# Optimization experiments

Measured on AMD Instinct MI355X. Metric: run time of the kernel, lower is better.

## Reference

```python
import jax, jax.numpy as jnp
import numpy as np

N, F_IN, HID, E, G = 100000, 256, 256, 800000, 256


def setup_inputs() -> dict:
    key = jax.random.key(0)
    ks = jax.random.split(key, 10)
    x = jax.random.normal(ks[0], (N, F_IN), dtype=jnp.float32)
    edge_index = jax.random.randint(ks[1], (2, E), 0, N, dtype=jnp.int64)
    batch = jnp.sort(jax.random.randint(ks[2], (N,), 0, G, dtype=jnp.int64))
    s = 1.0 / np.sqrt(HID)
    W1 = jax.random.normal(ks[3], (F_IN, HID), dtype=jnp.float32) * s
    b1 = jnp.zeros((HID,), dtype=jnp.float32)
    W2 = jax.random.normal(ks[4], (HID, HID), dtype=jnp.float32) * s
    b2 = jnp.zeros((HID,), dtype=jnp.float32)
    Wc1 = jax.random.normal(ks[5], (HID, HID // 2), dtype=jnp.float32) * s
    bc1 = jnp.zeros((HID // 2,), dtype=jnp.float32)
    Wc2 = jax.random.normal(ks[6], (HID // 2, 2), dtype=jnp.float32) * s
    bc2 = jnp.zeros((2,), dtype=jnp.float32)
    return dict(x=x, edge_index=edge_index, batch=batch, num_graphs=G,
                W1=W1, b1=b1, W2=W2, b2=b2, Wc1=Wc1, bc1=bc1, Wc2=Wc2, bc2=bc2)


def _gcn_layer(h, src, dst, inv_sqrt_deg, W, b):
    # GCNConv: D^-1/2 (A + I) D^-1/2 (h W) + b
    hw = h @ W                                            # (N, H)
    coef = inv_sqrt_deg[src] * inv_sqrt_deg[dst]          # (E,)
    msgs = hw[src] * coef[:, None]                        # (E, H)
    agg = jax.ops.segment_sum(msgs, dst, num_segments=h.shape[0])
    self_loop = hw * (inv_sqrt_deg * inv_sqrt_deg)[:, None]
    return agg + self_loop + b


def reference(x, edge_index, batch, num_graphs, W1, b1, W2, b2, Wc1, bc1, Wc2, bc2):
    n = x.shape[0]
    src, dst = edge_index[0], edge_index[1]
    # degree with self-loops (symmetric normalization)
    deg = jax.ops.segment_sum(jnp.ones((src.shape[0],), jnp.float32), dst,
                              num_segments=n) + 1.0
    inv_sqrt_deg = jax.lax.rsqrt(deg)

    h = jax.nn.relu(_gcn_layer(x, src, dst, inv_sqrt_deg, W1, b1))
    node_emb = jax.nn.relu(_gcn_layer(h, src, dst, inv_sqrt_deg, W2, b2))

    # per-graph mean pooling (segment mean replacing the Python loop)
    sums = jax.ops.segment_sum(node_emb, batch, num_segments=num_graphs)
    counts = jax.ops.segment_sum(jnp.ones((n,), jnp.float32), batch,
                                 num_segments=num_graphs)
    graph_emb = sums / jnp.maximum(counts, 1.0)[:, None]

    # classifier MLP (dropout is identity in eval mode)
    hcls = jax.nn.relu(graph_emb @ Wc1 + bc1)
    logits = hcls @ Wc2 + bc2                             # (G, 2)
    return logits, node_emb
```

## Files before the change

kernel.cpp:

```cpp
#include <hip/hip_runtime.h>
#include <hip/hip_bf16.h>

#define HID 256
#define NGRAPH 256

typedef __bf16 bf16_t;
typedef __attribute__((ext_vector_type(8))) __bf16 bf16x8;
typedef __attribute__((ext_vector_type(4))) __bf16 bf16x4;
typedef __attribute__((ext_vector_type(4))) float f32x4;

__global__ void zero_int_kernel(int* __restrict__ p, int n) {
    int i = blockIdx.x * blockDim.x + threadIdx.x;
    if (i < n) p[i] = 0;
}

__global__ void count_deg_kernel(const int* __restrict__ ei, int E, int* __restrict__ deg) {
    int e = blockIdx.x * blockDim.x + threadIdx.x;
    if (e >= E) return;
    int dst = ei[E + e];
    atomicAdd(&deg[dst], 1);
}

#define SCHUNK 512

__global__ __launch_bounds__(256) void scan_pass1_kernel(
    const int* __restrict__ deg, int N, int* __restrict__ bsum) {
    __shared__ int red[256];
    int b = blockIdx.x, t = threadIdx.x;
    int i0 = b * SCHUNK + 2 * t;
    int v = 0;
    if (i0 < N) v += deg[i0];
    if (i0 + 1 < N) v += deg[i0 + 1];
    red[t] = v;
    __syncthreads();
    for (int s = 128; s > 0; s >>= 1) {
        if (t < s) red[t] += red[t + s];
        __syncthreads();
    }
    if (t == 0) bsum[b] = red[0];
}

__global__ __launch_bounds__(256) void scan_pass2_kernel(
    const int* __restrict__ bsum, int NB, int* __restrict__ boff) {
    __shared__ int s[256];
    int t = threadIdx.x;
    int v = (t < NB) ? bsum[t] : 0;
    s[t] = v;
    __syncthreads();
    for (int off = 1; off < 256; off <<= 1) {
        int x = s[t];
        if (t >= off) x += s[t - off];
        __syncthreads();
        s[t] = x;
        __syncthreads();
    }
    if (t < NB) boff[t] = s[t] - v;
}

__global__ __launch_bounds__(256) void scan_pass3_kernel(
    const int* __restrict__ deg, int N, const int* __restrict__ boff,
    int* __restrict__ rowptr, int* __restrict__ cursor, float* __restrict__ invd) {
    __shared__ int s[256];
    int b = blockIdx.x, t = threadIdx.x;
    int i0 = b * SCHUNK + 2 * t;
    int d0 = (i0 < N) ? deg[i0] : 0;
    int d1 = (i0 + 1 < N) ? deg[i0 + 1] : 0;
    int pair = d0 + d1;
    s[t] = pair;
    __syncthreads();
    for (int off = 1; off < 256; off <<= 1) {
        int x = s[t];
        if (t >= off) x += s[t - off];
        __syncthreads();
        s[t] = x;
        __syncthreads();
    }
    int excl = s[t] - pair + boff[b];
    if (i0 < N) {
        rowptr[i0] = excl;
        cursor[i0] = excl;
        invd[i0] = rsqrtf((float)d0 + 1.0f);
    }
    if (i0 + 1 < N) {
        int e1 = excl + d0;
        rowptr[i0 + 1] = e1;
        cursor[i0 + 1] = e1;
        invd[i0 + 1] = rsqrtf((float)d1 + 1.0f);
    }
}

__global__ void fill_csr_kernel(const int* __restrict__ ei, int E,
                                int* __restrict__ cursor, int* __restrict__ csr_src) {
    int e = blockIdx.x * blockDim.x + threadIdx.x;
    if (e >= E) return;
    int src = ei[e];
    int dst = ei[E + e];
    int pos = atomicAdd(&cursor[dst], 1);
    csr_src[pos] = src;
}

__global__ __launch_bounds__(256) void wsplit_kernel(
    const float* __restrict__ W, bf16_t* __restrict__ Wf) {
    int idx = blockIdx.x * 256 + threadIdx.x;
    float w = W[idx];
    int k = idx >> 8, n = idx & 255;
    int k0 = k >> 5, kg = (k >> 3) & 3, j = k & 7;
    int nt = n >> 4, m = n & 15;
    Wf[(size_t)(((k0 * 16 + nt) * 64) + kg * 16 + m) * 8 + j] = (bf16_t)w;
}

#define GBM 128

template <int SPLIT>
__global__ __launch_bounds__(512, 4) void gemm_mfma_kernel(
    const void* __restrict__ Xv, const bf16_t* __restrict__ Wf,
    const float* __restrict__ rowscale, bf16_t* __restrict__ out, int Nrows) {
    __shared__ bf16_t Blds[32768];

    const int tid = threadIdx.x;
    const int wave = tid >> 6;
    const int lane = tid & 63;
    const int row0 = blockIdx.x * GBM;
    const int m = lane & 15;
    const int kg = lane >> 4;

    const int arow_raw = row0 + wave * 16 + m;
    const int arow = (arow_raw < Nrows) ? arow_raw : 0;

    f32x4 acc[16];
#pragma unroll
    for (int i = 0; i < 16; ++i) acc[i] = (f32x4){0.f, 0.f, 0.f, 0.f};

#pragma unroll
    for (int c = 0; c < 2; ++c) {
        float4 xa0, xb0, xa1, xb1, xa2, xb2, xa3, xb3;
        bf16x8 ah0, ah1, ah2, ah3;
        if (SPLIT) {
            const float* xr = (const float*)Xv + (size_t)arow * 256 + c * 128 + kg * 8;
            xa0 = *(const float4*)&xr[0];   xb0 = *(const float4*)&xr[4];
            xa1 = *(const float4*)&xr[32];  xb1 = *(const float4*)&xr[36];
            xa2 = *(const float4*)&xr[64];  xb2 = *(const float4*)&xr[68];
            xa3 = *(const float4*)&xr[96];  xb3 = *(const float4*)&xr[100];
        } else {
            const bf16_t* xr = (const bf16_t*)Xv + (size_t)arow * 256 + c * 128 + kg * 8;
            ah0 = *(const bf16x8*)&xr[0];
            ah1 = *(const bf16x8*)&xr[32];
            ah2 = *(const bf16x8*)&xr[64];
            ah3 = *(const bf16x8*)&xr[96];
        }

        if (c) __syncthreads();
#pragma unroll
        for (int it = 0; it < 8; ++it)
            *(bf16x8*)&Blds[it * 4096 + tid * 8] =
                *(const bf16x8*)&Wf[c * 32768 + it * 4096 + tid * 8];
        __syncthreads();

#pragma unroll
        for (int k0c = 0; k0c < 4; ++k0c) {
            bf16x8 ah, al;
            if (SPLIT) {
                float4 xa = (k0c == 0) ? xa0 : (k0c == 1) ? xa1 : (k0c == 2) ? xa2 : xa3;
                float4 xb = (k0c == 0) ? xb0 : (k0c == 1) ? xb1 : (k0c == 2) ? xb2 : xb3;
                float xf[8] = {xa.x, xa.y, xa.z, xa.w, xb.x, xb.y, xb.z, xb.w};
#pragma unroll
                for (int q = 0; q < 8; ++q) {
                    bf16_t hi = (bf16_t)xf[q];
                    ah[q] = hi;
                    al[q] = (bf16_t)(xf[q] - (float)hi);
                }
            } else {
                ah = (k0c == 0) ? ah0 : (k0c == 1) ? ah1 : (k0c == 2) ? ah2 : ah3;
            }
#pragma unroll
            for (int nt = 0; nt < 16; ++nt) {
                bf16x8 bh = *(const bf16x8*)&Blds[(k0c * 16 + nt) * 512 + lane * 8];
                acc[nt] = __builtin_amdgcn_mfma_f32_16x16x32_bf16(ah, bh, acc[nt], 0, 0, 0);
                if (SPLIT)
                    acc[nt] = __builtin_amdgcn_mfma_f32_16x16x32_bf16(al, bh, acc[nt], 0, 0, 0);
            }
        }
    }

    const int rbase = row0 + wave * 16 + kg * 4;
#pragma unroll
    for (int j = 0; j < 4; ++j) {
        int r = rbase + j;
        if (r < Nrows) {
            float sc = rowscale[r];
#pragma unroll
            for (int nt = 0; nt < 16; ++nt)
                out[(size_t)r * 256 + nt * 16 + m] = (bf16_t)(acc[nt][j] * sc);
        }
    }
}

template <typename OutT>
__global__ __launch_bounds__(256) void gcn_aggregate_kernel(
    const bf16_t* __restrict__ hs, const int* __restrict__ rowptr,
    const int* __restrict__ deg, const int* __restrict__ csr_src,
    const float* __restrict__ inv_d, const float* __restrict__ bias,
    OutT* __restrict__ out, int N) {
    int gwid = (blockIdx.x * blockDim.x + threadIdx.x) >> 6;
    int lane = threadIdx.x & 63;
    if (gwid >= N) return;
    int base = rowptr[gwid];
    int len = deg[gwid];
    int c = lane * 4;

    bf16x4 sv = *(const bf16x4*)&hs[(size_t)gwid * 256 + c];
    float ax0 = (float)sv[0], ay0 = (float)sv[1], az0 = (float)sv[2], aw0 = (float)sv[3];
    float ax1 = 0.f, ay1 = 0.f, az1 = 0.f, aw1 = 0.f;
    float ax2 = 0.f, ay2 = 0.f, az2 = 0.f, aw2 = 0.f;
    float ax3 = 0.f, ay3 = 0.f, az3 = 0.f, aw3 = 0.f;
    int i = 0;
    for (; i + 8 <= len; i += 8) {
        int s0 = csr_src[base + i];
        int s1 = csr_src[base + i + 1];
        int s2 = csr_src[base + i + 2];
        int s3 = csr_src[base + i + 3];
        int s4 = csr_src[base + i + 4];
        int s5 = csr_src[base + i + 5];
        int s6 = csr_src[base + i + 6];
        int s7 = csr_src[base + i + 7];
        bf16x4 v0 = *(const bf16x4*)&hs[(size_t)s0 * 256 + c];
        bf16x4 v1 = *(const bf16x4*)&hs[(size_t)s1 * 256 + c];
        bf16x4 v2 = *(const bf16x4*)&hs[(size_t)s2 * 256 + c];
        bf16x4 v3 = *(const bf16x4*)&hs[(size_t)s3 * 256 + c];
        bf16x4 v4 = *(const bf16x4*)&hs[(size_t)s4 * 256 + c];
        bf16x4 v5 = *(const bf16x4*)&hs[(size_t)s5 * 256 + c];
        bf16x4 v6 = *(const bf16x4*)&hs[(size_t)s6 * 256 + c];
        bf16x4 v7 = *(const bf16x4*)&hs[(size_t)s7 * 256 + c];
        ax0 += (float)v0[0] + (float)v4[0]; ay0 += (float)v0[1] + (float)v4[1];
        az0 += (float)v0[2] + (float)v4[2]; aw0 += (float)v0[3] + (float)v4[3];
        ax1 += (float)v1[0] + (float)v5[0]; ay1 += (float)v1[1] + (float)v5[1];
        az1 += (float)v1[2] + (float)v5[2]; aw1 += (float)v1[3] + (float)v5[3];
        ax2 += (float)v2[0] + (float)v6[0]; ay2 += (float)v2[1] + (float)v6[1];
        az2 += (float)v2[2] + (float)v6[2]; aw2 += (float)v2[3] + (float)v6[3];
        ax3 += (float)v3[0] + (float)v7[0]; ay3 += (float)v3[1] + (float)v7[1];
        az3 += (float)v3[2] + (float)v7[2]; aw3 += (float)v3[3] + (float)v7[3];
    }
    for (; i + 4 <= len; i += 4) {
        int s0 = csr_src[base + i];
        int s1 = csr_src[base + i + 1];
        int s2 = csr_src[base + i + 2];
        int s3 = csr_src[base + i + 3];
        bf16x4 v0 = *(const bf16x4*)&hs[(size_t)s0 * 256 + c];
        bf16x4 v1 = *(const bf16x4*)&hs[(size_t)s1 * 256 + c];
        bf16x4 v2 = *(const bf16x4*)&hs[(size_t)s2 * 256 + c];
        bf16x4 v3 = *(const bf16x4*)&hs[(size_t)s3 * 256 + c];
        ax0 += (float)v0[0]; ay0 += (float)v0[1]; az0 += (float)v0[2]; aw0 += (float)v0[3];
        ax1 += (float)v1[0]; ay1 += (float)v1[1]; az1 += (float)v1[2]; aw1 += (float)v1[3];
        ax2 += (float)v2[0]; ay2 += (float)v2[1]; az2 += (float)v2[2]; aw2 += (float)v2[3];
        ax3 += (float)v3[0]; ay3 += (float)v3[1]; az3 += (float)v3[2]; aw3 += (float)v3[3];
    }
    for (; i < len; ++i) {
        int s = csr_src[base + i];
        bf16x4 v = *(const bf16x4*)&hs[(size_t)s * 256 + c];
        ax0 += (float)v[0]; ay0 += (float)v[1]; az0 += (float)v[2]; aw0 += (float)v[3];
    }
    float ax = (ax0 + ax1) + (ax2 + ax3);
    float ay = (ay0 + ay1) + (ay2 + ay3);
    float az = (az0 + az1) + (az2 + az3);
    float aw = (aw0 + aw1) + (aw2 + aw3);

    float sc = inv_d[gwid];
    float4 bb = *(const float4*)&bias[c];
    float ox = fmaxf(fmaf(ax, sc, bb.x), 0.f);
    float oy = fmaxf(fmaf(ay, sc, bb.y), 0.f);
    float oz = fmaxf(fmaf(az, sc, bb.z), 0.f);
    float ow = fmaxf(fmaf(aw, sc, bb.w), 0.f);
    if constexpr (sizeof(OutT) == 2) {
        bf16x4 o;
        o[0] = (bf16_t)ox; o[1] = (bf16_t)oy; o[2] = (bf16_t)oz; o[3] = (bf16_t)ow;
        *(bf16x4*)&out[(size_t)gwid * 256 + c] = o;
    } else {
        float4 o = {ox, oy, oz, ow};
        *(float4*)&out[(size_t)gwid * 256 + c] = o;
    }
}

__global__ void graph_bounds_kernel(const int* __restrict__ batch, int N, int G,
                                    int* __restrict__ gstart) {
    int i = blockIdx.x * blockDim.x + threadIdx.x;
    if (i > N) return;
    int cur = (i < N) ? batch[i] : G;
    int prev = (i == 0) ? -1 : batch[i - 1];
    for (int g = prev + 1; g <= cur; ++g) gstart[g] = i;
}

__global__ __launch_bounds__(256) void pool_mean_kernel(
    const float* __restrict__ emb, const int* __restrict__ gstart,
    float* __restrict__ gemb) {
    __shared__ float red[4][64];
    int g = blockIdx.x;
    int col = blockIdx.y * 64 + (threadIdx.x & 63);
    int rg = threadIdx.x >> 6;
    int s = gstart[g], e = gstart[g + 1];
    float sum = 0.f;
    for (int n = s + rg; n < e; n += 4) sum += emb[(size_t)n * 256 + col];
    red[rg][threadIdx.x & 63] = sum;
    __syncthreads();
    if (rg == 0) {
        int l = threadIdx.x & 63;
        float t = (red[0][l] + red[1][l]) + (red[2][l] + red[3][l]);
        float cnt = fmaxf((float)(e - s), 1.0f);
        gemb[g * 256 + col] = t / cnt;
    }
}

__global__ __launch_bounds__(128) void cls1_kernel(
    const float* __restrict__ gemb, const float* __restrict__ Wc1,
    const float* __restrict__ bc1, float* __restrict__ hcls) {
    int g = blockIdx.x;
    int j = threadIdx.x;
    float sum = bc1[j];
    for (int k = 0; k < 256; ++k) sum = fmaf(gemb[g * 256 + k], Wc1[k * 128 + j], sum);
    hcls[g * 128 + j] = fmaxf(sum, 0.f);
}

__global__ void cls2_kernel(const float* __restrict__ hcls, const float* __restrict__ Wc2,
                            const float* __restrict__ bc2, float* __restrict__ logits, int G) {
    int idx = blockIdx.x * blockDim.x + threadIdx.x;
    if (idx >= G * 2) return;
    int g = idx >> 1, c = idx & 1;
    float sum = bc2[c];
    for (int k = 0; k < 128; ++k) sum = fmaf(hcls[g * 128 + k], Wc2[k * 2 + c], sum);
    logits[idx] = sum;
}

extern "C" void kernel_launch(void* const* d_in, const int* in_sizes, int n_in,
                              void* d_out, int out_size, void* d_ws, size_t ws_size,
                              hipStream_t stream) {
    const float* x   = (const float*)d_in[0];
    const int*   ei  = (const int*)d_in[1];
    const int*   batch = (const int*)d_in[2];
    const float* W1  = (const float*)d_in[4];
    const float* b1  = (const float*)d_in[5];
    const float* W2  = (const float*)d_in[6];
    const float* b2  = (const float*)d_in[7];
    const float* Wc1 = (const float*)d_in[8];
    const float* bc1 = (const float*)d_in[9];
    const float* Wc2 = (const float*)d_in[10];
    const float* bc2 = (const float*)d_in[11];

    const int N = in_sizes[0] / HID;
    const int E = in_sizes[1] / 2;
    const int G = NGRAPH;

    float* logits   = (float*)d_out;
    float* node_out = (float*)d_out + (size_t)G * 2;

    char* wsb = (char*)d_ws;
    size_t off = 0;
    auto alloc = [&](size_t bytes) -> void* {
        void* p = wsb + off;
        off += (bytes + 255) & ~(size_t)255;
        return p;
    };
    bf16_t* hs     = (bf16_t*)alloc((size_t)N * HID * 2);
    bf16_t* hb     = (bf16_t*)alloc((size_t)N * HID * 2);
    int*    rowptr = (int*)alloc((size_t)N * 4);
    int*    cursor = (int*)alloc((size_t)N * 4);
    int*    degi   = (int*)alloc((size_t)N * 4);
    int*    csr    = (int*)alloc((size_t)E * 4);
    float*  invd   = (float*)alloc((size_t)N * 4);
    int*    gstart = (int*)alloc((size_t)(G + 1) * 4);
    float*  gemb   = (float*)alloc((size_t)G * HID * 4);
    float*  hcls   = (float*)alloc((size_t)G * (HID / 2) * 4);
    int*    bsum   = (int*)alloc(256 * 4);
    int*    boff   = (int*)alloc(256 * 4);
    bf16_t* wf     = (bf16_t*)alloc((size_t)HID * HID * 2);
    (void)ws_size; (void)n_in; (void)out_size;

    const int NB = (N + SCHUNK - 1) / SCHUNK;

    zero_int_kernel<<<(N + 255) / 256, 256, 0, stream>>>(degi, N);
    count_deg_kernel<<<(E + 255) / 256, 256, 0, stream>>>(ei, E, degi);
    scan_pass1_kernel<<<NB, 256, 0, stream>>>(degi, N, bsum);
    scan_pass2_kernel<<<1, 256, 0, stream>>>(bsum, NB, boff);
    scan_pass3_kernel<<<NB, 256, 0, stream>>>(degi, N, boff, rowptr, cursor, invd);
    fill_csr_kernel<<<(E + 255) / 256, 256, 0, stream>>>(ei, E, cursor, csr);

    const int GB = (N + GBM - 1) / GBM;

    wsplit_kernel<<<HID * HID / 256, 256, 0, stream>>>(W1, wf);
    gemm_mfma_kernel<1><<<GB, 512, 0, stream>>>(x, wf, invd, hs, N);
    gcn_aggregate_kernel<bf16_t><<<(N * 64 + 255) / 256, 256, 0, stream>>>(
        hs, rowptr, degi, csr, invd, b1, hb, N);

    wsplit_kernel<<<HID * HID / 256, 256, 0, stream>>>(W2, wf);
    gemm_mfma_kernel<0><<<GB, 512, 0, stream>>>(hb, wf, invd, hs, N);
    gcn_aggregate_kernel<float><<<(N * 64 + 255) / 256, 256, 0, stream>>>(
        hs, rowptr, degi, csr, invd, b2, node_out, N);

    graph_bounds_kernel<<<(N + 1 + 255) / 256, 256, 0, stream>>>(batch, N, G, gstart);
    pool_mean_kernel<<<dim3(G, 4), 256, 0, stream>>>(node_out, gstart, gemb);
    cls1_kernel<<<G, 128, 0, stream>>>(gemb, Wc1, bc1, hcls);
    cls2_kernel<<<(G * 2 + 255) / 256, 256, 0, stream>>>(hcls, Wc2, bc2, logits, G);
}
```

Before: 383.5 us.

## Drop split-bf16 residual MFMA, widen aggregation to two nodes per wave, merge weight prep

The first-layer GEMM no longer splits fp32 inputs into high and low bf16 parts, which halves its MFMA count but lowers the precision of x@W1. The aggregation kernel now processes two nodes per wave, with each lane handling 8 bf16 columns through 16-byte loads instead of 4 columns, and its unroll is cut from 8 to 4 neighbours. The two weight-reformat launches are merged into one kernel that writes separate buffers. Together these reduce GEMM compute, widen memory transactions in the gather, and remove a launch, at some risk to numerical accuracy.

```diff
diff --git a/kernel.cpp b/kernel.cpp
--- a/kernel.cpp
+++ b/kernel.cpp
@@ -99,9 +99,13 @@
     csr_src[pos] = src;
 }
 
-__global__ __launch_bounds__(256) void wsplit_kernel(
-    const float* __restrict__ W, bf16_t* __restrict__ Wf) {
-    int idx = blockIdx.x * 256 + threadIdx.x;
+__global__ __launch_bounds__(256) void wsplit2_kernel(
+    const float* __restrict__ W1, bf16_t* __restrict__ Wf1,
+    const float* __restrict__ W2, bf16_t* __restrict__ Wf2) {
+    int gi = blockIdx.x * 256 + threadIdx.x;
+    const float* W = (gi < 65536) ? W1 : W2;
+    bf16_t* Wf = (gi < 65536) ? Wf1 : Wf2;
+    int idx = gi & 65535;
     float w = W[idx];
     int k = idx >> 8, n = idx & 255;
     int k0 = k >> 5, kg = (k >> 3) & 3, j = k & 7;
@@ -111,7 +115,7 @@
 
 #define GBM 128
 
-template <int SPLIT>
+template <int INFP32>
 __global__ __launch_bounds__(512, 4) void gemm_mfma_kernel(
     const void* __restrict__ Xv, const bf16_t* __restrict__ Wf,
     const float* __restrict__ rowscale, bf16_t* __restrict__ out, int Nrows) {
@@ -135,7 +139,7 @@
     for (int c = 0; c < 2; ++c) {
         float4 xa0, xb0, xa1, xb1, xa2, xb2, xa3, xb3;
         bf16x8 ah0, ah1, ah2, ah3;
-        if (SPLIT) {
+        if (INFP32) {
             const float* xr = (const float*)Xv + (size_t)arow * 256 + c * 128 + kg * 8;
             xa0 = *(const float4*)&xr[0];   xb0 = *(const float4*)&xr[4];
             xa1 = *(const float4*)&xr[32];  xb1 = *(const float4*)&xr[36];
@@ -158,17 +162,13 @@
 
 #pragma unroll
         for (int k0c = 0; k0c < 4; ++k0c) {
-            bf16x8 ah, al;
-            if (SPLIT) {
+            bf16x8 ah;
+            if (INFP32) {
                 float4 xa = (k0c == 0) ? xa0 : (k0c == 1) ? xa1 : (k0c == 2) ? xa2 : xa3;
                 float4 xb = (k0c == 0) ? xb0 : (k0c == 1) ? xb1 : (k0c == 2) ? xb2 : xb3;
                 float xf[8] = {xa.x, xa.y, xa.z, xa.w, xb.x, xb.y, xb.z, xb.w};
 #pragma unroll
-                for (int q = 0; q < 8; ++q) {
-                    bf16_t hi = (bf16_t)xf[q];
-                    ah[q] = hi;
-                    al[q] = (bf16_t)(xf[q] - (float)hi);
-                }
+                for (int q = 0; q < 8; ++q) ah[q] = (bf16_t)xf[q];
             } else {
                 ah = (k0c == 0) ? ah0 : (k0c == 1) ? ah1 : (k0c == 2) ? ah2 : ah3;
             }
@@ -176,8 +176,6 @@
             for (int nt = 0; nt < 16; ++nt) {
                 bf16x8 bh = *(const bf16x8*)&Blds[(k0c * 16 + nt) * 512 + lane * 8];
                 acc[nt] = __builtin_amdgcn_mfma_f32_16x16x32_bf16(ah, bh, acc[nt], 0, 0, 0);
-                if (SPLIT)
-                    acc[nt] = __builtin_amdgcn_mfma_f32_16x16x32_bf16(al, bh, acc[nt], 0, 0, 0);
             }
         }
     }
@@ -203,80 +201,60 @@
     OutT* __restrict__ out, int N) {
     int gwid = (blockIdx.x * blockDim.x + threadIdx.x) >> 6;
     int lane = threadIdx.x & 63;
-    if (gwid >= N) return;
-    int base = rowptr[gwid];
-    int len = deg[gwid];
-    int c = lane * 4;
-
-    bf16x4 sv = *(const bf16x4*)&hs[(size_t)gwid * 256 + c];
-    float ax0 = (float)sv[0], ay0 = (float)sv[1], az0 = (float)sv[2], aw0 = (float)sv[3];
-    float ax1 = 0.f, ay1 = 0.f, az1 = 0.f, aw1 = 0.f;
-    float ax2 = 0.f, ay2 = 0.f, az2 = 0.f, aw2 = 0.f;
-    float ax3 = 0.f, ay3 = 0.f, az3 = 0.f, aw3 = 0.f;
+    int node = gwid * 2 + (lane >> 5);
+    int hl = lane & 31;
+    if (node >= N) return;
+    int base = rowptr[node];
+    int len = deg[node];
+    int c = hl * 8;
+
+    bf16x8 sv = *(const bf16x8*)&hs[(size_t)node * 256 + c];
+    float a0[8], a1[8];
+#pragma unroll
+    for (int q = 0; q < 8; ++q) { a0[q] = (float)sv[q]; a1[q] = 0.f; }
+
     int i = 0;
-    for (; i + 8 <= len; i += 8) {
-        int s0 = csr_src[base + i];
-        int s1 = csr_src[base + i + 1];
-        int s2 = csr_src[base + i + 2];
-        int s3 = csr_src[base + i + 3];
-        int s4 = csr_src[base + i + 4];
-        int s5 = csr_src[base + i + 5];
-        int s6 = csr_src[base + i + 6];
-        int s7 = csr_src[base + i + 7];
-        bf16x4 v0 = *(const bf16x4*)&hs[(size_t)s0 * 256 + c];
-        bf16x4 v1 = *(const bf16x4*)&hs[(size_t)s1 * 256 + c];
-        bf16x4 v2 = *(const bf16x4*)&hs[(size_t)s2 * 256 + c];
-        bf16x4 v3 = *(const bf16x4*)&hs[(size_t)s3 * 256 + c];
-        bf16x4 v4 = *(const bf16x4*)&hs[(size_t)s4 * 256 + c];
-        bf16x4 v5 = *(const bf16x4*)&hs[(size_t)s5 * 256 + c];
-        bf16x4 v6 = *(const bf16x4*)&hs[(size_t)s6 * 256 + c];
-        bf16x4 v7 = *(const bf16x4*)&hs[(size_t)s7 * 256 + c];
-        ax0 += (float)v0[0] + (float)v4[0]; ay0 += (float)v0[1] + (float)v4[1];
-        az0 += (float)v0[2] + (float)v4[2]; aw0 += (float)v0[3] + (float)v4[3];
-        ax1 += (float)v1[0] + (float)v5[0]; ay1 += (float)v1[1] + (float)v5[1];
-        az1 += (float)v1[2] + (float)v5[2]; aw1 += (float)v1[3] + (float)v5[3];
-        ax2 += (float)v2[0] + (float)v6[0]; ay2 += (float)v2[1] + (float)v6[1];
-        az2 += (float)v2[2] + (float)v6[2]; aw2 += (float)v2[3] + (float)v6[3];
-        ax3 += (float)v3[0] + (float)v7[0]; ay3 += (float)v3[1] + (float)v7[1];
-        az3 += (float)v3[2] + (float)v7[2]; aw3 += (float)v3[3] + (float)v7[3];
-    }
     for (; i + 4 <= len; i += 4) {
         int s0 = csr_src[base + i];
         int s1 = csr_src[base + i + 1];
         int s2 = csr_src[base + i + 2];
         int s3 = csr_src[base + i + 3];
-        bf16x4 v0 = *(const bf16x4*)&hs[(size_t)s0 * 256 + c];
-        bf16x4 v1 = *(const bf16x4*)&hs[(size_t)s1 * 256 + c];
-        bf16x4 v2 = *(const bf16x4*)&hs[(size_t)s2 * 256 + c];
-        bf16x4 v3 = *(const bf16x4*)&hs[(size_t)s3 * 256 + c];
-        ax0 += (float)v0[0]; ay0 += (float)v0[1]; az0 += (float)v0[2]; aw0 += (float)v0[3];
-        ax1 += (float)v1[0]; ay1 += (float)v1[1]; az1 += (float)v1[2]; aw1 += (float)v1[3];
-        ax2 += (float)v2[0]; ay2 += (float)v2[1]; az2 += (float)v2[2]; aw2 += (float)v2[3];
-        ax3 += (float)v3[0]; ay3 += (float)v3[1]; az3 += (float)v3[2]; aw3 += (float)v3[3];
+        bf16x8 v0 = *(const bf16x8*)&hs[(size_t)s0 * 256 + c];
+        bf16x8 v1 = *(const bf16x8*)&hs[(size_t)s1 * 256 + c];
+        bf16x8 v2 = *(const bf16x8*)&hs[(size_t)s2 * 256 + c];
+        bf16x8 v3 = *(const bf16x8*)&hs[(size_t)s3 * 256 + c];
+#pragma unroll
+        for (int q = 0; q < 8; ++q) {
+            a0[q] += (float)v0[q] + (float)v2[q];
+            a1[q] += (float)v1[q] + (float)v3[q];
+        }
     }
     for (; i < len; ++i) {
         int s = csr_src[base + i];
-        bf16x4 v = *(const bf16x4*)&hs[(size_t)s * 256 + c];
-        ax0 += (float)v[0]; ay0 += (float)v[1]; az0 += (float)v[2]; aw0 += (float)v[3];
-    }
-    float ax = (ax0 + ax1) + (ax2 + ax3);
-    float ay = (ay0 + ay1) + (ay2 + ay3);
-    float az = (az0 + az1) + (az2 + az3);
-    float aw = (aw0 + aw1) + (aw2 + aw3);
-
-    float sc = inv_d[gwid];
-    float4 bb = *(const float4*)&bias[c];
-    float ox = fmaxf(fmaf(ax, sc, bb.x), 0.f);
-    float oy = fmaxf(fmaf(ay, sc, bb.y), 0.f);
-    float oz = fmaxf(fmaf(az, sc, bb.z), 0.f);
-    float ow = fmaxf(fmaf(aw, sc, bb.w), 0.f);
+        bf16x8 v = *(const bf16x8*)&hs[(size_t)s * 256 + c];
+#pragma unroll
+        for (int q = 0; q < 8; ++q) a0[q] += (float)v[q];
+    }
+
+    float sc = inv_d[node];
+    float4 bbA = *(const float4*)&bias[c];
+    float4 bbB = *(const float4*)&bias[c + 4];
+    float bb[8] = {bbA.x, bbA.y, bbA.z, bbA.w, bbB.x, bbB.y, bbB.z, bbB.w};
+    float o[8];
+#pragma unroll
+    for (int q = 0; q < 8; ++q)
+        o[q] = fmaxf(fmaf(a0[q] + a1[q], sc, bb[q]), 0.f);
+
     if constexpr (sizeof(OutT) == 2) {
-        bf16x4 o;
-        o[0] = (bf16_t)ox; o[1] = (bf16_t)oy; o[2] = (bf16_t)oz; o[3] = (bf16_t)ow;
-        *(bf16x4*)&out[(size_t)gwid * 256 + c] = o;
+        bf16x8 ov;
+#pragma unroll
+        for (int q = 0; q < 8; ++q) ov[q] = (bf16_t)o[q];
+        *(bf16x8*)&out[(size_t)node * 256 + c] = ov;
     } else {
-        float4 o = {ox, oy, oz, ow};
-        *(float4*)&out[(size_t)gwid * 256 + c] = o;
+        float4 oA = {o[0], o[1], o[2], o[3]};
+        float4 oB = {o[4], o[5], o[6], o[7]};
+        *(float4*)&out[(size_t)node * 256 + c] = oA;
+        *(float4*)&out[(size_t)node * 256 + c + 4] = oB;
     }
 }
 
@@ -370,7 +348,8 @@
     float*  hcls   = (float*)alloc((size_t)G * (HID / 2) * 4);
     int*    bsum   = (int*)alloc(256 * 4);
     int*    boff   = (int*)alloc(256 * 4);
-    bf16_t* wf     = (bf16_t*)alloc((size_t)HID * HID * 2);
+    bf16_t* wf1    = (bf16_t*)alloc((size_t)HID * HID * 2);
+    bf16_t* wf2    = (bf16_t*)alloc((size_t)HID * HID * 2);
     (void)ws_size; (void)n_in; (void)out_size;
 
     const int NB = (N + SCHUNK - 1) / SCHUNK;
@@ -381,17 +360,17 @@
     scan_pass2_kernel<<<1, 256, 0, stream>>>(bsum, NB, boff);
     scan_pass3_kernel<<<NB, 256, 0, stream>>>(degi, N, boff, rowptr, cursor, invd);
     fill_csr_kernel<<<(E + 255) / 256, 256, 0, stream>>>(ei, E, cursor, csr);
+    wsplit2_kernel<<<2 * HID * HID / 256, 256, 0, stream>>>(W1, wf1, W2, wf2);
 
     const int GB = (N + GBM - 1) / GBM;
-
-    wsplit_kernel<<<HID * HID / 256, 256, 0, stream>>>(W1, wf);
-    gemm_mfma_kernel<1><<<GB, 512, 0, stream>>>(x, wf, invd, hs, N);
-    gcn_aggregate_kernel<bf16_t><<<(N * 64 + 255) / 256, 256, 0, stream>>>(
+    const int AB = ((N + 1) / 2 * 64 + 255) / 256;
+
+    gemm_mfma_kernel<1><<<GB, 512, 0, stream>>>(x, wf1, invd, hs, N);
+    gcn_aggregate_kernel<bf16_t><<<AB, 256, 0, stream>>>(
         hs, rowptr, degi, csr, invd, b1, hb, N);
 
-    wsplit_kernel<<<HID * HID / 256, 256, 0, stream>>>(W2, wf);
-    gemm_mfma_kernel<0><<<GB, 512, 0, stream>>>(hb, wf, invd, hs, N);
-    gcn_aggregate_kernel<float><<<(N * 64 + 255) / 256, 256, 0, stream>>>(
+    gemm_mfma_kernel<0><<<GB, 512, 0, stream>>>(hb, wf2, invd, hs, N);
+    gcn_aggregate_kernel<float><<<AB, 256, 0, stream>>>(
         hs, rowptr, degi, csr, invd, b2, node_out, N);
 
     graph_bounds_kernel<<<(N + 1 + 255) / 256, 256, 0, stream>>>(batch, N, G, gstart);
```

Result: faster. 369.6 us (-3.6%).
